# Performance work log

Measured on AMD Instinct MI355X. Metric: run time of the kernel, lower is better.

Reference implementation:

```python
import jax, jax.numpy as jnp
import numpy as np

N, B, D = 100000, 1024, 768  # total nodes, num graphs, feature dim
DE = 64                      # placeholder edge-feat dim (unused, passed through)


def setup_inputs() -> dict:
    key = jax.random.key(0)
    ks = jax.random.split(key, 6)
    feat = jax.random.normal(ks[0], (N, D), jnp.float32)
    vn_feat = jax.random.normal(ks[1], (B, D), jnp.float32)
    edge_feat = jax.random.normal(ks[2], (B, DE), jnp.float32)
    batch = jnp.sort(jax.random.randint(ks[3], (N,), 0, B)).astype(jnp.int32)
    fc_W = jax.random.normal(ks[4], (D, D), jnp.float32) * 0.02
    fc_b = jnp.zeros((D,), jnp.float32)
    proj_W = jax.random.normal(ks[5], (D, D), jnp.float32) * 0.02
    proj_b = jnp.zeros((D,), jnp.float32)
    return dict(feat=feat, vn_feat=vn_feat, edge_feat=edge_feat, batch=batch,
                num_graphs=B, fc_W=fc_W, fc_b=fc_b, proj_W=proj_W, proj_b=proj_b)


def _logsum_pool(feat, batch, num_graphs):
    # r_i = (log N_i / N_i) * sum_k x_k  == mean_pool * log(num_nodes)
    seg_sum = jax.ops.segment_sum(feat, batch, num_segments=num_graphs)  # [B, D]
    cnt = jax.ops.segment_sum(jnp.ones((feat.shape[0],), feat.dtype), batch,
                              num_segments=num_graphs)                   # [B]
    cnt = jnp.maximum(cnt, 1.0)  # guard empty graphs (torch would NaN)
    return (seg_sum / cnt[:, None]) * jnp.log(cnt)[:, None]


def reference(feat, vn_feat, edge_feat, batch, num_graphs, fc_W, fc_b, proj_W, proj_b):
    # 1) scatter-pool node features per graph (logsum pooling)
    pool = _logsum_pool(feat, batch, num_graphs)            # [B, D]
    # 2) FCLayer: Linear -> (norm=none) -> relu -> (dropout=0)
    h = jax.nn.relu((pool + vn_feat) @ fc_W + fc_b)         # [B, D]
    # 3) residual virtual-node update
    vn_new = vn_feat + h                                    # [B, D]
    # 4) project and broadcast-add back to every node
    feat_out = feat + (vn_new @ proj_W + proj_b)[batch]     # [N, D]
    # use_edges=False: edge features pass through unchanged
    return feat_out, vn_new, edge_feat
```

## Files before the change

### kernel.cpp

```cpp
#include <hip/hip_runtime.h>
#include <cmath>

#define THREADS 256
#define PCOLS 192
#define T_RESIDENT 72000

typedef __attribute__((ext_vector_type(8))) short bf16x8;
typedef __attribute__((ext_vector_type(4))) float f32x4;

__device__ __forceinline__ short f2bf(float f) {
    return (short)(__builtin_bit_cast(unsigned, f) >> 16);
}

typedef const __attribute__((address_space(1))) unsigned int* gas1_t;
typedef __attribute__((address_space(3))) unsigned int* las3_t;
__device__ __forceinline__ void gload16(const short* g, short* l) {
    __builtin_amdgcn_global_load_lds((gas1_t)g, (las3_t)l, 16, 0, 0);
}

__device__ __forceinline__ int lower_bound_i(const int* __restrict__ arr, int n, int val) {
    int lo = 0, hi = n;
    while (lo < hi) {
        int mid = (lo + hi) >> 1;
        if (arr[mid] < val) lo = mid + 1; else hi = mid;
    }
    return lo;
}

__device__ __forceinline__ float4 f4add(float4 a, float4 b) {
    a.x += b.x; a.y += b.y; a.z += b.z; a.w += b.w; return a;
}
__device__ __forceinline__ float4 f4fma(float4 a, float s, float4 b) {
    b.x += a.x * s; b.y += a.y * s; b.z += a.z * s; b.w += a.w * s; return b;
}

template <bool NT>
__device__ __forceinline__ float4 ldf4(const float4* p) {
    if constexpr (NT) {
        f32x4 v = __builtin_nontemporal_load((const f32x4*)p);
        float4 r; r.x = v.x; r.y = v.y; r.z = v.z; r.w = v.w; return r;
    } else {
        return *p;
    }
}

__global__ void transpose_bf16(const float* __restrict__ src0, short* __restrict__ dst0,
                               const float* __restrict__ src1, short* __restrict__ dst1,
                               int n) {
    const float* src = blockIdx.z ? src1 : src0;
    short* dst = blockIdx.z ? dst1 : dst0;
    __shared__ short tile[32][33];
    int bx = blockIdx.x * 32, by = blockIdx.y * 32;
    int tx = threadIdx.x, ty = threadIdx.y;
    #pragma unroll
    for (int i = 0; i < 32; i += 8)
        tile[ty + i][tx] = f2bf(src[(size_t)(by + ty + i) * n + bx + tx]);
    __syncthreads();
    #pragma unroll
    for (int i = 0; i < 32; i += 8)
        dst[(size_t)(bx + ty + i) * n + by + tx] = tile[tx][ty + i];
}

template <bool NT>
__device__ __forceinline__ void accum8(const float4* __restrict__ base, int a, int b, int D4, int t,
                                       float4& a0, float4& a1, float4& a2, float4& a3,
                                       float4& a4, float4& a5, float4& a6, float4& a7) {
    const float4* __restrict__ p = base + (size_t)a * D4 + t;
    int r = a;
    for (; r + 8 <= b; r += 8) {
        float4 v0 = ldf4<NT>(p + 0 * (size_t)D4);
        float4 v1 = ldf4<NT>(p + 1 * (size_t)D4);
        float4 v2 = ldf4<NT>(p + 2 * (size_t)D4);
        float4 v3 = ldf4<NT>(p + 3 * (size_t)D4);
        float4 v4 = ldf4<NT>(p + 4 * (size_t)D4);
        float4 v5 = ldf4<NT>(p + 5 * (size_t)D4);
        float4 v6 = ldf4<NT>(p + 6 * (size_t)D4);
        float4 v7 = ldf4<NT>(p + 7 * (size_t)D4);
        a0 = f4add(a0, v0); a1 = f4add(a1, v1); a2 = f4add(a2, v2); a3 = f4add(a3, v3);
        a4 = f4add(a4, v4); a5 = f4add(a5, v5); a6 = f4add(a6, v6); a7 = f4add(a7, v7);
        p += 8 * (size_t)D4;
    }
    for (; r < b; ++r) {
        a0 = f4add(a0, ldf4<NT>(p));
        p += D4;
    }
}

__global__ void pool_kernel(const float4* __restrict__ feat4, const float4* __restrict__ vn4,
                            const int* __restrict__ batch, short* __restrict__ xbf,
                            int N, int D4, int Tres) {
    int g = blockIdx.x;
    __shared__ int s_range[2];
    if (threadIdx.x < 2) s_range[threadIdx.x] = lower_bound_i(batch, N, g + (int)threadIdx.x);
    __syncthreads();
    int lo = s_range[0], hi = s_range[1];
    int cnt = hi - lo;
    float scale = (cnt > 0) ? (logf((float)cnt) / (float)cnt) : 0.f;

    int t = threadIdx.x;
    float4 a0 = {0,0,0,0}, a1 = {0,0,0,0}, a2 = {0,0,0,0}, a3 = {0,0,0,0};
    float4 a4 = {0,0,0,0}, a5 = {0,0,0,0}, a6 = {0,0,0,0}, a7 = {0,0,0,0};

    int m = hi < Tres ? hi : (lo > Tres ? lo : Tres);
    accum8<false>(feat4, lo, m, D4, t, a0, a1, a2, a3, a4, a5, a6, a7);
    accum8<true >(feat4, m, hi, D4, t, a0, a1, a2, a3, a4, a5, a6, a7);

    float4 s = f4add(f4add(f4add(a0, a1), f4add(a2, a3)), f4add(f4add(a4, a5), f4add(a6, a7)));
    float4 vnv = vn4[(size_t)g * D4 + t];
    float4 x = f4fma(s, scale, vnv);
    short4 o;
    o.x = f2bf(x.x); o.y = f2bf(x.y); o.z = f2bf(x.z); o.w = f2bf(x.w);
    *(short4*)(xbf + ((size_t)g * D4 + t) * 4) = o;
}

template <bool RELU, bool ADD_RES, bool WRITE_BF>
__global__ __launch_bounds__(256) void gemm_bf(const short* __restrict__ A,
        const short* __restrict__ Wt, const float* __restrict__ bias,
        const float* __restrict__ res, float* __restrict__ out,
        short* __restrict__ out_bf, int Nn, int K) {
    __shared__ short lds[2][2][64 * 32];
    const int tid = threadIdx.x;
    const int lane = tid & 63;
    const int wid = tid >> 6;
    const int wr = wid >> 1, wc = wid & 1;
    const int lrow = lane & 15;
    const int kg = lane >> 4;
    const int tileM = blockIdx.y * 64;
    const int tileN = blockIdx.x * 64;
    const int nk = K / 32;

    f32x4 acc[2][2] = {};

    const int srow = tid >> 2;
    const int sci = (tid & 3) ^ (srow & 3);

    #define STG(buf, kt) do {                                                    \
        short* La = lds[buf][0];                                                 \
        short* Lb = lds[buf][1];                                                 \
        gload16(A  + (size_t)(tileM + srow) * K + (kt) * 32 + sci * 8, La + tid * 8); \
        gload16(Wt + (size_t)(tileN + srow) * K + (kt) * 32 + sci * 8, Lb + tid * 8); \
    } while (0)

    STG(0, 0);
    __syncthreads();

    for (int kt = 0; kt < nk; ++kt) {
        if (kt + 1 < nk) STG((kt + 1) & 1, kt + 1);
        const short* La = lds[kt & 1][0];
        const short* Lb = lds[kt & 1][1];
        bf16x8 a[2], b[2];
        #pragma unroll
        for (int m = 0; m < 2; ++m) {
            int row = wr * 32 + m * 16 + lrow;
            a[m] = *(const bf16x8*)(La + row * 32 + ((kg ^ (row & 3)) * 8));
        }
        #pragma unroll
        for (int n = 0; n < 2; ++n) {
            int col = wc * 32 + n * 16 + lrow;
            b[n] = *(const bf16x8*)(Lb + col * 32 + ((kg ^ (col & 3)) * 8));
        }
        #pragma unroll
        for (int m = 0; m < 2; ++m)
            #pragma unroll
            for (int n = 0; n < 2; ++n)
                acc[m][n] = __builtin_amdgcn_mfma_f32_16x16x32_bf16(a[m], b[n], acc[m][n], 0, 0, 0);
        __syncthreads();
    }

    #pragma unroll
    for (int m = 0; m < 2; ++m) {
        #pragma unroll
        for (int n = 0; n < 2; ++n) {
            int col = tileN + wc * 32 + n * 16 + lrow;
            float bv = bias[col];
            #pragma unroll
            for (int r = 0; r < 4; ++r) {
                int row = tileM + wr * 32 + m * 16 + kg * 4 + r;
                float v = acc[m][n][r] + bv;
                if (RELU) v = fmaxf(v, 0.f);
                if (ADD_RES) v += res[(size_t)row * Nn + col];
                out[(size_t)row * Nn + col] = v;
                if (WRITE_BF) out_bf[(size_t)row * Nn + col] = f2bf(v);
            }
        }
    }
    #undef STG
}

__global__ void node_add_kernel(const float4* __restrict__ feat4, const float4* __restrict__ y4,
                                const int* __restrict__ batch, float* __restrict__ out,
                                int N, int D4, int Tres) {
    int node = (int)(blockIdx.x * blockDim.y + threadIdx.y);
    if (node >= N) return;
    int t = threadIdx.x;
    int b = batch[node];
    size_t idx = (size_t)node * D4 + t;
    float4 f = (node < Tres) ? feat4[idx] : ldf4<true>(&feat4[idx]);
    float4 v = y4[(size_t)b * D4 + t];
    f32x4 r;
    r.x = f.x + v.x; r.y = f.y + v.y; r.z = f.z + v.z; r.w = f.w + v.w;
    __builtin_nontemporal_store(r, (f32x4*)(out + idx * 4));
}

extern "C" void kernel_launch(void* const* d_in, const int* in_sizes, int n_in,
                              void* d_out, int out_size, void* d_ws, size_t ws_size,
                              hipStream_t stream) {
    const float* feat  = (const float*)d_in[0];
    const float* vn    = (const float*)d_in[1];
    const float* edge  = (const float*)d_in[2];
    const int*   batch = (const int*)d_in[3];
    const float* fcW   = (const float*)d_in[5];
    const float* fcb   = (const float*)d_in[6];
    const float* pW    = (const float*)d_in[7];
    const float* pb    = (const float*)d_in[8];

    const int D = in_sizes[6];
    const int N = in_sizes[0] / D;
    const int B = in_sizes[1] / D;
    const int edge_elems = in_sizes[2];
    const int D4 = D / 4;

    float* out_feat = (float*)d_out;
    float* out_vn   = out_feat + (size_t)N * D;
    float* out_edge = out_vn + (size_t)B * D;

    char* ws = (char*)d_ws;
    size_t off = 0;
    short* xbf  = (short*)(ws + off); off += (size_t)B * D * 2;
    short* x2bf = (short*)(ws + off); off += (size_t)B * D * 2;
    short* fcWt = (short*)(ws + off); off += (size_t)D * D * 2;
    short* pWt  = (short*)(ws + off); off += (size_t)D * D * 2;
    float* y    = (float*)(ws + off);

    dim3 tb(32, 8);
    dim3 tg(D / 32, D / 32, 2);
    transpose_bf16<<<tg, tb, 0, stream>>>(fcW, fcWt, pW, pWt, D);

    pool_kernel<<<B, PCOLS, 0, stream>>>((const float4*)feat, (const float4*)vn,
                                         batch, xbf, N, D4, T_RESIDENT);

    dim3 gdim(D / 64, B / 64);
    gemm_bf<true, true, true><<<gdim, THREADS, 0, stream>>>(xbf, fcWt, fcb, vn,
                                                            out_vn, x2bf, D, D);

    gemm_bf<false, false, false><<<gdim, THREADS, 0, stream>>>(x2bf, pWt, pb, nullptr,
                                                               y, nullptr, D, D);

    dim3 nblk(192, 2);
    node_add_kernel<<<(N + 1) / 2, nblk, 0, stream>>>((const float4*)feat, (const float4*)y,
                                                      batch, out_feat, N, D4, T_RESIDENT);

    hipMemcpyAsync(out_edge, edge, (size_t)edge_elems * sizeof(float),
                   hipMemcpyDeviceToDevice, stream);
}
```

Before: 182.6 us.

## Fold edge copy into prep kernel and process node pairs in reverse order

```diff
diff --git a/kernel.cpp b/kernel.cpp
--- a/kernel.cpp
+++ b/kernel.cpp
@@ -44,9 +44,17 @@
     }
 }
 
-__global__ void transpose_bf16(const float* __restrict__ src0, short* __restrict__ dst0,
-                               const float* __restrict__ src1, short* __restrict__ dst1,
-                               int n) {
+__global__ void prep_kernel(const float* __restrict__ src0, short* __restrict__ dst0,
+                            const float* __restrict__ src1, short* __restrict__ dst1,
+                            int n, const float4* __restrict__ edge4,
+                            float4* __restrict__ out_edge4, int edge_elems4) {
+    if (blockIdx.z == 2) {
+        int fb = blockIdx.y * gridDim.x + blockIdx.x;
+        int t = threadIdx.y * 32 + threadIdx.x;
+        int i = fb * 256 + t;
+        if (i < edge_elems4) out_edge4[i] = edge4[i];
+        return;
+    }
     const float* src = blockIdx.z ? src1 : src0;
     short* dst = blockIdx.z ? dst1 : dst0;
     __shared__ short tile[32][33];
@@ -190,16 +198,35 @@
 __global__ void node_add_kernel(const float4* __restrict__ feat4, const float4* __restrict__ y4,
                                 const int* __restrict__ batch, float* __restrict__ out,
                                 int N, int D4, int Tres) {
-    int node = (int)(blockIdx.x * blockDim.y + threadIdx.y);
-    if (node >= N) return;
+    int idx = (int)(blockIdx.x * (blockDim.y * 2) + threadIdx.y * 2);
+    int na = N - 1 - idx;
+    if (na < 0) return;
+    int nb = na - 1;
     int t = threadIdx.x;
-    int b = batch[node];
-    size_t idx = (size_t)node * D4 + t;
-    float4 f = (node < Tres) ? feat4[idx] : ldf4<true>(&feat4[idx]);
-    float4 v = y4[(size_t)b * D4 + t];
-    f32x4 r;
-    r.x = f.x + v.x; r.y = f.y + v.y; r.z = f.z + v.z; r.w = f.w + v.w;
-    __builtin_nontemporal_store(r, (f32x4*)(out + idx * 4));
+
+    int ba = batch[na];
+    size_t ia = (size_t)na * D4 + t;
+    float4 fa = (na < Tres) ? feat4[ia] : ldf4<true>(&feat4[ia]);
+    float4 va = y4[(size_t)ba * D4 + t];
+
+    bool hb = (nb >= 0);
+    float4 fb = {0,0,0,0}, vb = {0,0,0,0};
+    size_t ib = 0;
+    if (hb) {
+        int bb = batch[nb];
+        ib = (size_t)nb * D4 + t;
+        fb = (nb < Tres) ? feat4[ib] : ldf4<true>(&feat4[ib]);
+        vb = y4[(size_t)bb * D4 + t];
+    }
+
+    f32x4 ra;
+    ra.x = fa.x + va.x; ra.y = fa.y + va.y; ra.z = fa.z + va.z; ra.w = fa.w + va.w;
+    __builtin_nontemporal_store(ra, (f32x4*)(out + ia * 4));
+    if (hb) {
+        f32x4 rb;
+        rb.x = fb.x + vb.x; rb.y = fb.y + vb.y; rb.z = fb.z + vb.z; rb.w = fb.w + vb.w;
+        __builtin_nontemporal_store(rb, (f32x4*)(out + ib * 4));
+    }
 }
 
 extern "C" void kernel_launch(void* const* d_in, const int* in_sizes, int n_in,
@@ -233,8 +260,10 @@
     float* y    = (float*)(ws + off);
 
     dim3 tb(32, 8);
-    dim3 tg(D / 32, D / 32, 2);
-    transpose_bf16<<<tg, tb, 0, stream>>>(fcW, fcWt, pW, pWt, D);
+    dim3 tg(D / 32, D / 32, 3);
+    prep_kernel<<<tg, tb, 0, stream>>>(fcW, fcWt, pW, pWt, D,
+                                       (const float4*)edge, (float4*)out_edge,
+                                       edge_elems / 4);
 
     pool_kernel<<<B, PCOLS, 0, stream>>>((const float4*)feat, (const float4*)vn,
                                          batch, xbf, N, D4, T_RESIDENT);
@@ -247,9 +276,6 @@
                                                                y, nullptr, D, D);
 
     dim3 nblk(192, 2);
-    node_add_kernel<<<(N + 1) / 2, nblk, 0, stream>>>((const float4*)feat, (const float4*)y,
+    node_add_kernel<<<(N + 3) / 4, nblk, 0, stream>>>((const float4*)feat, (const float4*)y,
                                                       batch, out_feat, N, D4, T_RESIDENT);
-
-    hipMemcpyAsync(out_edge, edge, (size_t)edge_elems * sizeof(float),
-                   hipMemcpyDeviceToDevice, stream);
-}
+}
```

New measurement: 175.2 us. 1.04x faster.
